# Kernel optimization log

Measured on AMD Instinct MI355X. Metric: run time of the kernel, lower is better.

Reference implementation:

```python
import jax, jax.numpy as jnp
import numpy as np
import math

B, CIN, CH, H, W = 4, 64, 32, 64, 64
M_CH, DEPTH, K = 4, 3, 8
NPF = CIN // 2  # num_pos_feats per axis; pos channels = 2*NPF = CIN
TEMPERATURE = 10000.0


def sine_pos(h, w, npf, temperature=TEMPERATURE):
    # PositionEmbeddingSine with normalize=False; cumsum of ones == arange(1, n+1)
    y_embed = jnp.arange(1, h + 1, dtype=jnp.float32)
    x_embed = jnp.arange(1, w + 1, dtype=jnp.float32)
    dim_t = jnp.arange(npf, dtype=jnp.float32)
    dim_t = temperature ** (2.0 * jnp.floor(dim_t / 2.0) / npf)
    pos_x = jnp.broadcast_to(x_embed[None, :, None] / dim_t, (h, w, npf))
    pos_y = jnp.broadcast_to(y_embed[:, None, None] / dim_t, (h, w, npf))

    def interleave(p):
        return jnp.stack([jnp.sin(p[..., 0::2]), jnp.cos(p[..., 1::2])], axis=-1).reshape(h, w, npf)

    pos = jnp.concatenate([interleave(pos_y), interleave(pos_x)], axis=-1)  # (h,w,2*npf)
    return jnp.transpose(pos, (2, 0, 1))  # (2*npf, h, w)


def conv2d(x, wgt, bias, pad):
    y = jax.lax.conv_general_dilated(
        x, wgt, window_strides=(1, 1), padding=[(pad, pad), (pad, pad)],
        dimension_numbers=('NCHW', 'OIHW', 'NCHW'))
    return y + bias[None, :, None, None]


def setup_inputs() -> dict:
    key = jax.random.key(0)
    ks = jax.random.split(key, 13)
    s = 0.05
    return {
        'f':    jax.random.normal(ks[0], (B, CH, H, W), jnp.float32),
        'map':  jax.random.normal(ks[1], (B, 1, 32, 32), jnp.float32),
        'f_q':  jax.random.normal(ks[2], (B, CIN, H, W), jnp.float32),
        'f_k':  jax.random.normal(ks[3], (B, CIN, H, W), jnp.float32),
        'm_k':  jax.random.normal(ks[4], (B, 1, 32, 32), jnp.float32),
        'wq':   jax.random.normal(ks[5], (M_CH, CIN), jnp.float32) * s,
        'wk':   jax.random.normal(ks[6], (M_CH, CIN), jnp.float32) * s,
        'w_in':  jax.random.normal(ks[7], (CH, CH, 1, 1), jnp.float32) * s,
        'b_in':  jax.random.normal(ks[8], (CH,), jnp.float32) * s,
        'w_mid': jax.random.normal(ks[9], (DEPTH, CH, CH, 3, 3), jnp.float32) * s,
        'b_mid': jax.random.normal(ks[10], (DEPTH, CH), jnp.float32) * s,
        'w_out': jax.random.normal(ks[11], (1, CH, 3, 3), jnp.float32) * s,
        'b_out': jax.random.normal(ks[12], (1,), jnp.float32) * s,
    }


def reference(f, map, f_q, f_k, m_k, wq, wk, w_in, b_in, w_mid, b_mid, w_out, b_out):
    b, c, h, w = f_q.shape
    hf, wf = f.shape[2], f.shape[3]
    # self.ret: bilinear resize to f's spatial size (align_corners=False)
    map_r = jax.image.resize(map, (b, 1, hf, wf), method='bilinear')
    m_k_r = jax.image.resize(m_k, (b, 1, hf, wf), method='bilinear')

    pos = sine_pos(h, w, NPF)[None]  # (1, CIN, h, w); same for pos_emb_h/pos_emb_l
    fq_emb = f_q + pos
    fk_emb = f_k + pos

    # 1x1 convs == channel matmuls
    query = jnp.einsum('mc,bchw->bhwm', wq, fq_emb).reshape(b, h * w, M_CH)  # (b, N, m)
    key_t = jnp.einsum('mc,bchw->bmhw', wk, fk_emb).reshape(b, M_CH, h * w)  # (b, m, N)

    sim = jnp.einsum('bqm,bmk->bqk', query, key_t)   # (b, N, N)
    sim = jax.nn.softmax(sim, axis=-2)                # softmax over query axis (dim=-2)

    value = (jnp.exp(m_k_r) / math.e).reshape(b, 1, h * w)  # broadcast over query axis
    context = sim * value
    context_k, _ = jax.lax.top_k(context, K)          # (b, N, K) over last (key) axis
    context_m = jnp.mean(context_k, axis=-1)          # (b, N)
    corrected_map = context_m.reshape(b, 1, h, w)

    corrected_map = corrected_map * map_r + map_r
    rmap = 1.0 - jax.nn.sigmoid(corrected_map)

    x = rmap * f  # broadcast over channel dim
    x = conv2d(x, w_in, b_in, 0)
    for i in range(DEPTH):
        x = jax.nn.relu(conv2d(x, w_mid[i], b_mid[i], 1))
    out = conv2d(x, w_out, b_out, 1) + corrected_map
    return (x, out, corrected_map)
```

## Files before the change

### kernel.cpp

```cpp
#include <hip/hip_runtime.h>
#include <hip/hip_bf16.h>
#include <math.h>

#define BB 4
#define CIN 64
#define CH 32
#define HH 64
#define WW 64
#define NN 4096
#define MCH 4
#define NQCH 32
#define LOG2E 1.4426950408889634f

#define PP_OFF     0
#define Q4_OFF     1024
#define K4_OFF     66560
#define CV_OFF     132096
#define CPSUM_OFF  672768
#define RMAP_OFF   148480
#define CMAPF_OFF  164864
#define T8_OFF     181248
#define XA_OFF     181248
#define XB_OFF     705536

#define OUT_X_OFF   0
#define OUT_O_OFF   524288
#define OUT_CM_OFF  540672

#define CE(x, y) { float ce_lo = fminf(x, y); y = fmaxf(x, y); x = ce_lo; }

__device__ __forceinline__ float bilin32(const float* src, int b, int y, int x) {
    float sy = 0.5f * y - 0.25f;
    float sx = 0.5f * x - 0.25f;
    float fy0 = floorf(sy), fx0 = floorf(sx);
    int y0 = (int)fy0, x0 = (int)fx0;
    float fy = sy - fy0, fx = sx - fx0;
    int y0c = min(max(y0, 0), 31), y1c = min(max(y0 + 1, 0), 31);
    int x0c = min(max(x0, 0), 31), x1c = min(max(x0 + 1, 0), 31);
    const float* p = src + b * 1024;
    float v00 = p[y0c * 32 + x0c], v01 = p[y0c * 32 + x1c];
    float v10 = p[y1c * 32 + x0c], v11 = p[y1c * 32 + x1c];
    float v0 = v00 + fx * (v01 - v00);
    float v1 = v10 + fx * (v11 - v10);
    return v0 + fy * (v1 - v0);
}

__global__ void k0_posproj(const float* __restrict__ wq, const float* __restrict__ wk,
                           float* __restrict__ pp) {
    int t = threadIdx.x;
    float coord = (float)(t + 1);
    float qy[4] = {0,0,0,0}, qx[4] = {0,0,0,0}, ky[4] = {0,0,0,0}, kx[4] = {0,0,0,0};
    for (int c = 0; c < 32; ++c) {
        float e = (2.0f * (float)(c / 2)) / 32.0f;
        float dim = powf(10000.0f, e);
        float ang = coord / dim;
        float pr = (c & 1) ? cosf(ang) : sinf(ang);
        #pragma unroll
        for (int m = 0; m < 4; ++m) {
            qy[m] += wq[m * 64 + c] * pr;
            qx[m] += wq[m * 64 + 32 + c] * pr;
            ky[m] += wk[m * 64 + c] * pr;
            kx[m] += wk[m * 64 + 32 + c] * pr;
        }
    }
    #pragma unroll
    for (int m = 0; m < 4; ++m) {
        pp[0 * 256 + m * 64 + t] = qy[m];
        pp[1 * 256 + m * 64 + t] = qx[m];
        pp[2 * 256 + m * 64 + t] = ky[m];
        pp[3 * 256 + m * 64 + t] = kx[m];
    }
}

__global__ __launch_bounds__(512) void k1_qk(
        const float* __restrict__ fq, const float* __restrict__ fk,
        const float* __restrict__ wq, const float* __restrict__ wk,
        const float* __restrict__ pp,
        float* __restrict__ Q4, float* __restrict__ K4) {
    __shared__ float wqs[256], wks[256];
    __shared__ float red[512][9];
    int tid = threadIdx.x;
    if (tid < 256) { wqs[tid] = wq[tid]; wks[tid] = wk[tid]; }
    __syncthreads();
    int qi = tid & 63, g = tid >> 6;
    int gid = blockIdx.x * 64 + qi;
    int b = gid >> 12, hw = gid & 4095;
    const float* fqb = fq + (size_t)b * CIN * NN + hw;
    const float* fkb = fk + (size_t)b * CIN * NN + hw;
    float aq[4] = {0,0,0,0}, ak[4] = {0,0,0,0};
    int c0 = g * 8;
    #pragma unroll
    for (int c = c0; c < c0 + 8; ++c) {
        float vq = fqb[c * NN];
        float vk = fkb[c * NN];
        #pragma unroll
        for (int m = 0; m < 4; ++m) {
            aq[m] += wqs[m * 64 + c] * vq;
            ak[m] += wks[m * 64 + c] * vk;
        }
    }
    #pragma unroll
    for (int m = 0; m < 4; ++m) { red[tid][m] = aq[m]; red[tid][4 + m] = ak[m]; }
    __syncthreads();
    if (tid < 64) {
        int y = hw >> 6, x = hw & 63;
        float q4[4], k4[4];
        #pragma unroll
        for (int m = 0; m < 4; ++m) {
            float sq = 0.0f, sk = 0.0f;
            #pragma unroll
            for (int j = 0; j < 8; ++j) {
                sq += red[tid + 64 * j][m];
                sk += red[tid + 64 * j][4 + m];
            }
            q4[m] = LOG2E * (sq + pp[0 * 256 + m * 64 + y] + pp[1 * 256 + m * 64 + x]);
            k4[m] = sk + pp[2 * 256 + m * 64 + y] + pp[3 * 256 + m * 64 + x];
        }
        ((float4*)Q4)[gid] = make_float4(q4[0], q4[1], q4[2], q4[3]);
        ((float4*)K4)[gid] = make_float4(k4[0], k4[1], k4[2], k4[3]);
    }
}

__global__ void k2a_colstats(const float* __restrict__ Q4, const float* __restrict__ K4,
                             float* __restrict__ cpsum) {
    int blk = blockIdx.x;
    int kblk = blk & 7;   blk >>= 3;
    int qch  = blk & 31;  blk >>= 5;
    int b    = blk;
    int tid = threadIdx.x;
    const float4* Qg = (const float4*)Q4 + b * NN + qch * 128;
    int k0 = kblk * 512 + tid;
    float4 kva = ((const float4*)K4)[b * NN + k0];
    float4 kvb = ((const float4*)K4)[b * NN + k0 + 256];
    float sa = 0.0f, sb = 0.0f;
    #pragma unroll 8
    for (int i = 0; i < 128; ++i) {
        float4 q = Qg[i];
        float da = fmaf(q.x, kva.x, fmaf(q.y, kva.y, fmaf(q.z, kva.z, q.w * kva.w)));
        float db = fmaf(q.x, kvb.x, fmaf(q.y, kvb.y, fmaf(q.z, kvb.z, q.w * kvb.w)));
        sa += exp2f(da);
        sb += exp2f(db);
    }
    cpsum[(b * NQCH + qch) * NN + k0] = sa;
    cpsum[(b * NQCH + qch) * NN + k0 + 256] = sb;
}

__global__ void k2b_cmerge(const float* __restrict__ cpsum,
                           const float* __restrict__ m_k, float* __restrict__ cvals) {
    int gid = blockIdx.x * 256 + threadIdx.x;
    int b = gid >> 12, k = gid & 4095;
    float S = 0.0f;
    #pragma unroll
    for (int j = 0; j < NQCH; ++j) S += cpsum[(b * NQCH + j) * NN + k];
    float mk = bilin32(m_k, b, k >> 6, k & 63);
    cvals[gid] = LOG2E * (mk - 1.0f) - log2f(S);
}

__global__ __launch_bounds__(256) void k3a_scan(
        const float* __restrict__ Q4, const float* __restrict__ K4,
        const float* __restrict__ cvals, float* __restrict__ t8) {
    int blk = blockIdx.x;
    int kc = blk & 7;   blk >>= 3;
    int g4 = blk & 15;  blk >>= 4;
    int b  = blk;
    int tid = threadIdx.x;
    int wave = tid >> 6, lane = tid & 63;
    int qrow = (g4 * 4 + wave) * 64 + lane;
    float4 qv = ((const float4*)Q4)[b * NN + qrow];
    const float4* Kb = (const float4*)K4 + b * NN + kc * 512;
    const float* cb = cvals + b * NN + kc * 512;

    float t0=-1e30f,t1=-1e30f,t2=-1e30f,t3=-1e30f;
    float t4=-1e30f,t5=-1e30f,t6=-1e30f,t7=-1e30f;

    #pragma unroll 2
    for (int i0 = 0; i0 < 512; i0 += 8) {
        float4 k0 = Kb[i0 + 0]; float4 k1 = Kb[i0 + 1];
        float4 k2 = Kb[i0 + 2]; float4 k3 = Kb[i0 + 3];
        float4 k4 = Kb[i0 + 4]; float4 k5 = Kb[i0 + 5];
        float4 k6 = Kb[i0 + 6]; float4 k7 = Kb[i0 + 7];
        float s0 = fmaf(qv.x,k0.x, fmaf(qv.y,k0.y, fmaf(qv.z,k0.z, qv.w*k0.w))) + cb[i0+0];
        float s1 = fmaf(qv.x,k1.x, fmaf(qv.y,k1.y, fmaf(qv.z,k1.z, qv.w*k1.w))) + cb[i0+1];
        float s2 = fmaf(qv.x,k2.x, fmaf(qv.y,k2.y, fmaf(qv.z,k2.z, qv.w*k2.w))) + cb[i0+2];
        float s3 = fmaf(qv.x,k3.x, fmaf(qv.y,k3.y, fmaf(qv.z,k3.z, qv.w*k3.w))) + cb[i0+3];
        float s4 = fmaf(qv.x,k4.x, fmaf(qv.y,k4.y, fmaf(qv.z,k4.z, qv.w*k4.w))) + cb[i0+4];
        float s5 = fmaf(qv.x,k5.x, fmaf(qv.y,k5.y, fmaf(qv.z,k5.z, qv.w*k5.w))) + cb[i0+5];
        float s6 = fmaf(qv.x,k6.x, fmaf(qv.y,k6.y, fmaf(qv.z,k6.z, qv.w*k6.w))) + cb[i0+6];
        float s7 = fmaf(qv.x,k7.x, fmaf(qv.y,k7.y, fmaf(qv.z,k7.z, qv.w*k7.w))) + cb[i0+7];
        float bm = fmaxf(fmaxf(fmaxf(s0,s1), fmaxf(s2,s3)),
                         fmaxf(fmaxf(s4,s5), fmaxf(s6,s7)));
        if (bm > t0) {
            CE(s0,s1); CE(s2,s3); CE(s4,s5); CE(s6,s7);
            CE(s0,s2); CE(s1,s3); CE(s4,s6); CE(s5,s7);
            CE(s1,s2); CE(s5,s6);
            CE(s0,s4); CE(s1,s5); CE(s2,s6); CE(s3,s7);
            CE(s2,s4); CE(s3,s5);
            CE(s1,s2); CE(s3,s4); CE(s5,s6);
            t0 = fmaxf(t0, s7); t1 = fmaxf(t1, s6); t2 = fmaxf(t2, s5); t3 = fmaxf(t3, s4);
            t4 = fmaxf(t4, s3); t5 = fmaxf(t5, s2); t6 = fmaxf(t6, s1); t7 = fmaxf(t7, s0);
            CE(t0,t4); CE(t1,t5); CE(t2,t6); CE(t3,t7);
            CE(t0,t2); CE(t1,t3); CE(t4,t6); CE(t5,t7);
            CE(t0,t1); CE(t2,t3); CE(t4,t5); CE(t6,t7);
        }
    }
    float* o = t8 + ((size_t)(b * NN + qrow)) * 64 + kc * 8;
    o[0] = t0; o[1] = t1; o[2] = t2; o[3] = t3;
    o[4] = t4; o[5] = t5; o[6] = t6; o[7] = t7;
}

__global__ void k3b_merge(const float* __restrict__ t8, const float* __restrict__ mapin,
                          float* __restrict__ rmap, float* __restrict__ cmapf,
                          float* __restrict__ outp) {
    int tid = threadIdx.x;
    int qid = blockIdx.x * 4 + (tid >> 6);
    int lane = tid & 63;
    float v = t8[(size_t)qid * 64 + lane];
    float sm = 0.0f;
    #pragma unroll
    for (int r = 0; r < 8; ++r) {
        float m = v;
        int ln = lane;
        #pragma unroll
        for (int off = 32; off >= 1; off >>= 1) {
            float om = __shfl_xor(m, off);
            int ol = __shfl_xor(ln, off);
            if (om > m || (om == m && ol < ln)) { m = om; ln = ol; }
        }
        sm += exp2f(m);
        if (lane == ln) v = -1e30f;
    }
    if (lane == 0) {
        float cmv = sm * 0.125f;
        int b = qid >> 12, hw = qid & 4095;
        float mr = bilin32(mapin, b, hw >> 6, hw & 63);
        float cm = cmv * mr + mr;
        float rm = 1.0f / (1.0f + __expf(cm));
        rmap[qid] = rm;
        cmapf[qid] = cm;
        outp[OUT_CM_OFF + qid] = cm;
    }
}

__global__ void k4_conv1(const float* __restrict__ f, const float* __restrict__ rmap,
                         const float* __restrict__ w_in, const float* __restrict__ b_in,
                         float* __restrict__ xout) {
    __shared__ float ws_[1024];
    __shared__ float bs[32];
    int tid = threadIdx.x;
    for (int i = tid; i < 1024; i += 256) ws_[i] = w_in[i];
    if (tid < 32) bs[tid] = b_in[tid];
    __syncthreads();
    int gid = blockIdx.x * 256 + tid;
    int hw = gid & 4095;
    int og = (gid >> 12) & 7;
    int b  = gid >> 15;
    float rm = rmap[b * NN + hw];
    float acc[4];
    #pragma unroll
    for (int j = 0; j < 4; ++j) acc[j] = bs[og * 4 + j];
    const float* fb = f + (size_t)b * CH * NN + hw;
    for (int i = 0; i < 32; ++i) {
        float v = fb[i * NN] * rm;
        #pragma unroll
        for (int j = 0; j < 4; ++j) acc[j] += ws_[(og * 4 + j) * 32 + i] * v;
    }
    float* xo = xout + (size_t)b * CH * NN + (og * 4) * NN + hw;
    #pragma unroll
    for (int j = 0; j < 4; ++j) xo[j * NN] = acc[j];
}

__global__ void k5_conv3(const float* __restrict__ xin, const float* __restrict__ w,
                         const float* __restrict__ bias, float* __restrict__ xout,
                         float* __restrict__ outx) {
    __shared__ float tile[32][324];
    __shared__ float wsm[1152];
    __shared__ float bsm[4];
    int blk = blockIdx.x;
    int og = blk & 7;  blk >>= 3;
    int tx = blk & 3;  blk >>= 2;
    int ty = blk & 3;  blk >>= 2;
    int b  = blk;
    int tid = threadIdx.x;
    for (int i = tid; i < 1152; i += 256) wsm[i] = w[og * 1152 + i];
    if (tid < 4) bsm[tid] = bias[og * 4 + tid];
    int y0 = ty * 16 - 1, x0 = tx * 16 - 1;
    for (int i = tid; i < 32 * 324; i += 256) {
        int c = i / 324, r = i % 324;
        int yy = r / 18, xx = r % 18;
        int gy = y0 + yy, gx = x0 + xx;
        float v = 0.0f;
        if (gy >= 0 && gy < 64 && gx >= 0 && gx < 64)
            v = xin[((size_t)b * CH + c) * NN + gy * 64 + gx];
        tile[c][r] = v;
    }
    __syncthreads();
    int py = tid >> 4, px = tid & 15;
    float acc[4];
    #pragma unroll
    for (int j = 0; j < 4; ++j) acc[j] = bsm[j];
    for (int i = 0; i < 32; ++i) {
        const float* tr = &tile[i][py * 18 + px];
        float v00 = tr[0],  v01 = tr[1],  v02 = tr[2];
        float v10 = tr[18], v11 = tr[19], v12 = tr[20];
        float v20 = tr[36], v21 = tr[37], v22 = tr[38];
        #pragma unroll
        for (int j = 0; j < 4; ++j) {
            const float* wj = &wsm[j * 288 + i * 9];
            acc[j] += v00 * wj[0] + v01 * wj[1] + v02 * wj[2]
                    + v10 * wj[3] + v11 * wj[4] + v12 * wj[5]
                    + v20 * wj[6] + v21 * wj[7] + v22 * wj[8];
        }
    }
    size_t base = (size_t)b * CH * NN + (size_t)(og * 4) * NN
                + (ty * 16 + py) * 64 + tx * 16 + px;
    #pragma unroll
    for (int j = 0; j < 4; ++j) {
        float r_ = fmaxf(acc[j], 0.0f);
        xout[base + j * NN] = r_;
        if (outx) outx[base + j * NN] = r_;
    }
}

__global__ void k6_convout(const float* __restrict__ xin, const float* __restrict__ w_out,
                           const float* __restrict__ b_out, const float* __restrict__ cmapf,
                           float* __restrict__ outp) {
    __shared__ float wsm[288];
    __shared__ float red[256];
    int tid = threadIdx.x;
    for (int i = tid; i < 288; i += 256) wsm[i] = w_out[i];
    int pxi = tid & 63, g = tid >> 6;
    int gid = blockIdx.x * 64 + pxi;
    int b = gid >> 12, hw = gid & 4095;
    int y = hw >> 6, x = hw & 63;
    __syncthreads();
    float acc = 0.0f;
    int c0 = g * 8;
    for (int i = c0; i < c0 + 8; ++i) {
        const float* xi = xin + ((size_t)b * CH + i) * NN;
        #pragma unroll
        for (int ky = 0; ky < 3; ++ky) {
            int gy = y + ky - 1;
            if (gy < 0 || gy > 63) continue;
            #pragma unroll
            for (int kx = 0; kx < 3; ++kx) {
                int gx = x + kx - 1;
                if (gx < 0 || gx > 63) continue;
                acc += xi[gy * 64 + gx] * wsm[i * 9 + ky * 3 + kx];
            }
        }
    }
    red[tid] = acc;
    __syncthreads();
    if (tid < 64) {
        float a = red[tid] + red[tid + 64] + red[tid + 128] + red[tid + 192]
                + b_out[0] + cmapf[gid];
        outp[OUT_O_OFF + gid] = a;
    }
}

extern "C" void kernel_launch(void* const* d_in, const int* in_sizes, int n_in,
                              void* d_out, int out_size, void* d_ws, size_t ws_size,
                              hipStream_t stream) {
    const float* f     = (const float*)d_in[0];
    const float* mapin = (const float*)d_in[1];
    const float* f_q   = (const float*)d_in[2];
    const float* f_k   = (const float*)d_in[3];
    const float* m_k   = (const float*)d_in[4];
    const float* wq    = (const float*)d_in[5];
    const float* wk    = (const float*)d_in[6];
    const float* w_in  = (const float*)d_in[7];
    const float* b_in  = (const float*)d_in[8];
    const float* w_mid = (const float*)d_in[9];
    const float* b_mid = (const float*)d_in[10];
    const float* w_out = (const float*)d_in[11];
    const float* b_out = (const float*)d_in[12];
    float* outp = (float*)d_out;
    float* ws = (float*)d_ws;

    float* PP    = ws + PP_OFF;
    float* Q4    = ws + Q4_OFF;
    float* K4    = ws + K4_OFF;
    float* CV    = ws + CV_OFF;
    float* CPSUM = ws + CPSUM_OFF;
    float* RMAP  = ws + RMAP_OFF;
    float* CMAPF = ws + CMAPF_OFF;
    float* T8    = ws + T8_OFF;
    float* XA    = ws + XA_OFF;
    float* XB    = ws + XB_OFF;

    k0_posproj<<<1, 64, 0, stream>>>(wq, wk, PP);
    k1_qk<<<256, 512, 0, stream>>>(f_q, f_k, wq, wk, PP, Q4, K4);
    k2a_colstats<<<BB * NQCH * 8, 256, 0, stream>>>(Q4, K4, CPSUM);
    k2b_cmerge<<<64, 256, 0, stream>>>(CPSUM, m_k, CV);
    k3a_scan<<<BB * 16 * 8, 256, 0, stream>>>(Q4, K4, CV, T8);
    k3b_merge<<<BB * NN / 4, 256, 0, stream>>>(T8, mapin, RMAP, CMAPF, outp);
    k4_conv1<<<512, 256, 0, stream>>>(f, RMAP, w_in, b_in, XA);
    k5_conv3<<<512, 256, 0, stream>>>(XA, w_mid + 0 * 9216, b_mid + 0 * 32, XB, (float*)0);
    k5_conv3<<<512, 256, 0, stream>>>(XB, w_mid + 1 * 9216, b_mid + 1 * 32, XA, (float*)0);
    k5_conv3<<<512, 256, 0, stream>>>(XA, w_mid + 2 * 9216, b_mid + 2 * 32, XB, outp + OUT_X_OFF);
    k6_convout<<<256, 256, 0, stream>>>(XB, w_out, b_out, CMAPF, outp);
}
```

Measured before the change: 223.5 us.

## Fuse positional projection into QK kernel and split top-k scan into more chunks

Removes the single-block positional-projection kernel launch. Each QK block now recomputes the projection into shared memory, with powf replaced by exp2f. The top-k scan is split into 16 key chunks instead of 8, doubling the grid to raise parallelism. The merge kernel now handles 128 partial candidates per query by holding two values per lane, and the CPSUM buffer is moved to overlap the T8/XA region. The trade-offs are redundant trig work in every QK block and twice the partial top-k traffic.

```diff
diff --git a/kernel.cpp b/kernel.cpp
--- a/kernel.cpp
+++ b/kernel.cpp
@@ -11,15 +11,15 @@
 #define MCH 4
 #define NQCH 32
 #define LOG2E 1.4426950408889634f
-
-#define PP_OFF     0
+#define L2_10K 13.287712379549449f
+
 #define Q4_OFF     1024
 #define K4_OFF     66560
 #define CV_OFF     132096
-#define CPSUM_OFF  672768
 #define RMAP_OFF   148480
 #define CMAPF_OFF  164864
 #define T8_OFF     181248
+#define CPSUM_OFF  181248
 #define XA_OFF     181248
 #define XB_OFF     705536
 
@@ -45,43 +45,41 @@
     return v0 + fy * (v1 - v0);
 }
 
-__global__ void k0_posproj(const float* __restrict__ wq, const float* __restrict__ wk,
-                           float* __restrict__ pp) {
-    int t = threadIdx.x;
-    float coord = (float)(t + 1);
-    float qy[4] = {0,0,0,0}, qx[4] = {0,0,0,0}, ky[4] = {0,0,0,0}, kx[4] = {0,0,0,0};
-    for (int c = 0; c < 32; ++c) {
-        float e = (2.0f * (float)(c / 2)) / 32.0f;
-        float dim = powf(10000.0f, e);
-        float ang = coord / dim;
-        float pr = (c & 1) ? cosf(ang) : sinf(ang);
-        #pragma unroll
-        for (int m = 0; m < 4; ++m) {
-            qy[m] += wq[m * 64 + c] * pr;
-            qx[m] += wq[m * 64 + 32 + c] * pr;
-            ky[m] += wk[m * 64 + c] * pr;
-            kx[m] += wk[m * 64 + 32 + c] * pr;
-        }
-    }
-    #pragma unroll
-    for (int m = 0; m < 4; ++m) {
-        pp[0 * 256 + m * 64 + t] = qy[m];
-        pp[1 * 256 + m * 64 + t] = qx[m];
-        pp[2 * 256 + m * 64 + t] = ky[m];
-        pp[3 * 256 + m * 64 + t] = kx[m];
-    }
-}
-
 __global__ __launch_bounds__(512) void k1_qk(
         const float* __restrict__ fq, const float* __restrict__ fk,
         const float* __restrict__ wq, const float* __restrict__ wk,
-        const float* __restrict__ pp,
         float* __restrict__ Q4, float* __restrict__ K4) {
     __shared__ float wqs[256], wks[256];
+    __shared__ float pp[1024];
     __shared__ float red[512][9];
     int tid = threadIdx.x;
     if (tid < 256) { wqs[tid] = wq[tid]; wks[tid] = wk[tid]; }
     __syncthreads();
+
+    if (tid < 64) {
+        float coord = (float)(tid + 1);
+        float qy[4] = {0,0,0,0}, qx[4] = {0,0,0,0}, ky[4] = {0,0,0,0}, kx[4] = {0,0,0,0};
+        for (int c = 0; c < 32; ++c) {
+            float e = (2.0f * (float)(c >> 1)) * (1.0f / 32.0f);
+            float ang = coord * exp2f(-e * L2_10K);
+            float pr = (c & 1) ? cosf(ang) : sinf(ang);
+            #pragma unroll
+            for (int m = 0; m < 4; ++m) {
+                qy[m] += wqs[m * 64 + c] * pr;
+                qx[m] += wqs[m * 64 + 32 + c] * pr;
+                ky[m] += wks[m * 64 + c] * pr;
+                kx[m] += wks[m * 64 + 32 + c] * pr;
+            }
+        }
+        #pragma unroll
+        for (int m = 0; m < 4; ++m) {
+            pp[0 * 256 + m * 64 + tid] = qy[m];
+            pp[1 * 256 + m * 64 + tid] = qx[m];
+            pp[2 * 256 + m * 64 + tid] = ky[m];
+            pp[3 * 256 + m * 64 + tid] = kx[m];
+        }
+    }
+
     int qi = tid & 63, g = tid >> 6;
     int gid = blockIdx.x * 64 + qi;
     int b = gid >> 12, hw = gid & 4095;
@@ -160,21 +158,21 @@
         const float* __restrict__ Q4, const float* __restrict__ K4,
         const float* __restrict__ cvals, float* __restrict__ t8) {
     int blk = blockIdx.x;
-    int kc = blk & 7;   blk >>= 3;
+    int kc = blk & 15;  blk >>= 4;
     int g4 = blk & 15;  blk >>= 4;
     int b  = blk;
     int tid = threadIdx.x;
     int wave = tid >> 6, lane = tid & 63;
     int qrow = (g4 * 4 + wave) * 64 + lane;
     float4 qv = ((const float4*)Q4)[b * NN + qrow];
-    const float4* Kb = (const float4*)K4 + b * NN + kc * 512;
-    const float* cb = cvals + b * NN + kc * 512;
+    const float4* Kb = (const float4*)K4 + b * NN + kc * 256;
+    const float* cb = cvals + b * NN + kc * 256;
 
     float t0=-1e30f,t1=-1e30f,t2=-1e30f,t3=-1e30f;
     float t4=-1e30f,t5=-1e30f,t6=-1e30f,t7=-1e30f;
 
     #pragma unroll 2
-    for (int i0 = 0; i0 < 512; i0 += 8) {
+    for (int i0 = 0; i0 < 256; i0 += 8) {
         float4 k0 = Kb[i0 + 0]; float4 k1 = Kb[i0 + 1];
         float4 k2 = Kb[i0 + 2]; float4 k3 = Kb[i0 + 3];
         float4 k4 = Kb[i0 + 4]; float4 k5 = Kb[i0 + 5];
@@ -203,7 +201,7 @@
             CE(t0,t1); CE(t2,t3); CE(t4,t5); CE(t6,t7);
         }
     }
-    float* o = t8 + ((size_t)(b * NN + qrow)) * 64 + kc * 8;
+    float* o = t8 + ((size_t)(b * NN + qrow)) * 128 + kc * 8;
     o[0] = t0; o[1] = t1; o[2] = t2; o[3] = t3;
     o[4] = t4; o[5] = t5; o[6] = t6; o[7] = t7;
 }
@@ -214,11 +212,13 @@
     int tid = threadIdx.x;
     int qid = blockIdx.x * 4 + (tid >> 6);
     int lane = tid & 63;
-    float v = t8[(size_t)qid * 64 + lane];
+    float va = t8[(size_t)qid * 128 + lane];
+    float vb = t8[(size_t)qid * 128 + 64 + lane];
+    float hi = fmaxf(va, vb), lo = fminf(va, vb);
     float sm = 0.0f;
     #pragma unroll
     for (int r = 0; r < 8; ++r) {
-        float m = v;
+        float m = hi;
         int ln = lane;
         #pragma unroll
         for (int off = 32; off >= 1; off >>= 1) {
@@ -227,7 +227,7 @@
             if (om > m || (om == m && ol < ln)) { m = om; ln = ol; }
         }
         sm += exp2f(m);
-        if (lane == ln) v = -1e30f;
+        if (lane == ln) { hi = lo; lo = -1e30f; }
     }
     if (lane == 0) {
         float cmv = sm * 0.125f;
@@ -377,7 +377,6 @@
     float* outp = (float*)d_out;
     float* ws = (float*)d_ws;
 
-    float* PP    = ws + PP_OFF;
     float* Q4    = ws + Q4_OFF;
     float* K4    = ws + K4_OFF;
     float* CV    = ws + CV_OFF;
@@ -388,11 +387,10 @@
     float* XA    = ws + XA_OFF;
     float* XB    = ws + XB_OFF;
 
-    k0_posproj<<<1, 64, 0, stream>>>(wq, wk, PP);
-    k1_qk<<<256, 512, 0, stream>>>(f_q, f_k, wq, wk, PP, Q4, K4);
+    k1_qk<<<256, 512, 0, stream>>>(f_q, f_k, wq, wk, Q4, K4);
     k2a_colstats<<<BB * NQCH * 8, 256, 0, stream>>>(Q4, K4, CPSUM);
     k2b_cmerge<<<64, 256, 0, stream>>>(CPSUM, m_k, CV);
-    k3a_scan<<<BB * 16 * 8, 256, 0, stream>>>(Q4, K4, CV, T8);
+    k3a_scan<<<BB * 16 * 16, 256, 0, stream>>>(Q4, K4, CV, T8);
     k3b_merge<<<BB * NN / 4, 256, 0, stream>>>(T8, mapin, RMAP, CMAPF, outp);
     k4_conv1<<<512, 256, 0, stream>>>(f, RMAP, w_in, b_in, XA);
     k5_conv3<<<512, 256, 0, stream>>>(XA, w_mid + 0 * 9216, b_mid + 0 * 32, XB, (float*)0);
```

New measurement: 206.4 us. 1.08x faster.
